# Optimization experiments

Hardware: AMD Instinct MI355X
Metric: run time of the kernel (lower is better)

## Reference

```python
import jax, jax.numpy as jnp
import numpy as np


def fps(p, m):
    """Furthest point sampling. p: (B,N,3) -> idx (B,m) int32. Starts at index 0 like pointops."""
    p = jax.lax.stop_gradient(p)
    B, N, _ = p.shape
    d2 = jnp.full((B, N), jnp.inf, dtype=p.dtype)  # min sq-dist to selected set
    first = jnp.zeros((B,), dtype=jnp.int32)

    def step(carry, _):
        d2, last = carry
        lastp = jnp.take_along_axis(p, last[:, None, None].astype(jnp.int32), axis=1)  # (B,1,3)
        dist = jnp.sum((p - lastp) ** 2, axis=-1)  # (B,N)
        d2 = jnp.minimum(d2, dist)
        nxt = jnp.argmax(d2, axis=-1).astype(jnp.int32)
        return (d2, nxt), last

    _, idx = jax.lax.scan(step, (d2, first), None, length=m)
    return jnp.transpose(idx)  # (B,m)


def knn_indices(p1, p2, k):
    """k nearest neighbors of p2 (B,M,3) among p1 (B,N,3) -> (B,M,k) int32."""
    p1 = jax.lax.stop_gradient(p1)
    p2 = jax.lax.stop_gradient(p2)
    # squared distances (B,M,N)
    d2 = (jnp.sum(p2 ** 2, -1)[:, :, None]
          + jnp.sum(p1 ** 2, -1)[:, None, :]
          - 2.0 * jnp.einsum('bmd,bnd->bmn', p2, p1))
    _, idx = jax.lax.top_k(-d2, k)
    return idx.astype(jnp.int32)


def setup_inputs() -> dict:
    key = jax.random.key(0)
    k1, k2 = jax.random.split(key)
    B, N, C = 8, 8192, 64
    p1 = jax.random.normal(k1, (B, N, 3), dtype=jnp.float32)
    x = jax.random.normal(k2, (B, N, C), dtype=jnp.float32)
    return {"p1": p1, "x": x, "stride": 4, "num_neighbors": 16}


def reference(p1, x, stride, num_neighbors):
    B, N, C = x.shape
    M = N // stride
    idx = fps(p1, M)                                   # (B,M) int32
    p2 = jnp.take_along_axis(p1, idx[:, :, None], 1)   # (B,M,3) sampled coords
    nn = knn_indices(p1, p2, num_neighbors)            # (B,M,k)
    # gather features: (B,M,k,C)
    grouped = jax.vmap(lambda xb, ib: xb[ib])(x, nn)
    y = jnp.mean(grouped, axis=2)                      # (B,M,C)
    return (y, p2, idx)
```

## Files before the change

### kernel.cpp

```cpp
#include <hip/hip_runtime.h>

#define Bn 8
#define Nn 8192
#define Cn 64
#define Mn 2048
#define Kn 16
#define FPS_T 512
#define PPT (Nn / FPS_T)

template <int CTRL, int RMASK>
__device__ __forceinline__ float dpp_max_step(float v) {
    int mv = __builtin_amdgcn_update_dpp(__float_as_int(v), __float_as_int(v),
                                         CTRL, RMASK, 0xF, false);
    return fmaxf(v, __int_as_float(mv));
}
template <int CTRL, int RMASK>
__device__ __forceinline__ unsigned dpp_min_step(unsigned v) {
    unsigned mv = (unsigned)__builtin_amdgcn_update_dpp((int)v, (int)v,
                                                        CTRL, RMASK, 0xF, false);
    return (mv < v) ? mv : v;
}
__device__ __forceinline__ float wave_max_f32(float v) {
    v = dpp_max_step<0x111, 0xF>(v);
    v = dpp_max_step<0x112, 0xF>(v);
    v = dpp_max_step<0x114, 0xF>(v);
    v = dpp_max_step<0x118, 0xF>(v);
    v = dpp_max_step<0x142, 0xA>(v);
    v = dpp_max_step<0x143, 0xC>(v);
    return v;
}
__device__ __forceinline__ unsigned wave_min_u32(unsigned v) {
    v = dpp_min_step<0x111, 0xF>(v);
    v = dpp_min_step<0x112, 0xF>(v);
    v = dpp_min_step<0x114, 0xF>(v);
    v = dpp_min_step<0x118, 0xF>(v);
    v = dpp_min_step<0x142, 0xA>(v);
    v = dpp_min_step<0x143, 0xC>(v);
    return v;
}

__global__ __launch_bounds__(FPS_T) void fps_kernel(
    const float* __restrict__ p1,
    float* __restrict__ out_p2,
    float* __restrict__ out_idxf)
{
    __shared__ float s_Px[Nn], s_Py[Nn], s_Pz[Nn];
    __shared__ unsigned long long s_key[3];
    __shared__ int s_oidx[Mn];

    const int b = blockIdx.x;
    const int t = threadIdx.x;
    const float* __restrict__ P = p1 + (size_t)b * (Nn * 3);

    float px[PPT], py[PPT], pz[PPT], d2[PPT];
#pragma unroll
    for (int j = 0; j < PPT; ++j) {
        const int g = t + j * FPS_T;
        const float x = P[g * 3 + 0];
        const float y = P[g * 3 + 1];
        const float z = P[g * 3 + 2];
        px[j] = x; py[j] = y; pz[j] = z;
        s_Px[g] = x; s_Py[g] = y; s_Pz[g] = z;
        d2[j] = __int_as_float(0x7f800000);
    }
    if (t < 3) s_key[t] = 0ull;
    if (t == 0) s_oidx[0] = 0;
    __syncthreads();

    float qx = s_Px[0], qy = s_Py[0], qz = s_Pz[0];

    for (int m = 1; m < Mn; ++m) {
        float lm = -1.0f;
#pragma unroll
        for (int j = 0; j < PPT; ++j) {
            const float dx = __fsub_rn(px[j], qx);
            const float dy = __fsub_rn(py[j], qy);
            const float dz = __fsub_rn(pz[j], qz);
            const float dist = __fadd_rn(
                __fadd_rn(__fmul_rn(dx, dx), __fmul_rn(dy, dy)),
                __fmul_rn(dz, dz));
            const float nd = fminf(d2[j], dist);
            d2[j] = nd;
            lm = fmaxf(lm, nd);
        }
        lm = wave_max_f32(lm);
        const float V = __int_as_float(
            __builtin_amdgcn_readlane(__float_as_int(lm), 63));
        unsigned cand = 0xFFFFFFFFu;
#pragma unroll
        for (int j = PPT - 1; j >= 0; --j)
            cand = (d2[j] == V) ? (unsigned)(t + j * FPS_T) : cand;
        cand = wave_min_u32(cand);
        if ((t & 63) == 63) {
            const unsigned long long key =
                ((unsigned long long)(unsigned)__float_as_int(V) << 32) |
                (unsigned long long)(~cand);
            atomicMax(&s_key[m % 3], key);
        }
        if (t == 0) s_key[(m + 1) % 3] = 0ull;
        __syncthreads();
        const unsigned long long key = s_key[m % 3];
        const int bi = (int)(~(unsigned)key);
        if (t == 0) s_oidx[m] = bi;
        qx = s_Px[bi]; qy = s_Py[bi]; qz = s_Pz[bi];
    }
    __syncthreads();

    float* __restrict__ o2 = out_p2 + (size_t)b * Mn * 3;
    float* __restrict__ oi = out_idxf + (size_t)b * Mn;
    for (int i = t; i < Mn; i += FPS_T) {
        const int bi = s_oidx[i];
        oi[i] = (float)bi;
        o2[i * 3 + 0] = s_Px[bi];
        o2[i * 3 + 1] = s_Py[bi];
        o2[i * 3 + 2] = s_Pz[bi];
    }
}

#define KNN_WPB 4
__global__ __launch_bounds__(64 * KNN_WPB) void knn_mean_kernel(
    const float* __restrict__ p1,
    const float* __restrict__ x,
    const float* __restrict__ p2,
    float* __restrict__ y)
{
    const int lane = threadIdx.x & 63;
    const int wid  = threadIdx.x >> 6;
    const int q    = blockIdx.x * KNN_WPB + wid;
    const int b    = q >> 11;
    const float* __restrict__ P = p1 + (size_t)b * (Nn * 3);

    const float qx = p2[(size_t)q * 3 + 0];
    const float qy = p2[(size_t)q * 3 + 1];
    const float qz = p2[(size_t)q * 3 + 2];
    const float qq = __fadd_rn(
        __fadd_rn(__fmul_rn(qx, qx), __fmul_rn(qy, qy)), __fmul_rn(qz, qz));

    float slotv = __int_as_float(0x7f800000);
    int   sloti = 0x7fffffff;
    float thr   = __int_as_float(0x7f800000);
    int   thri  = 0x7fffffff;

    for (int c = 0; c < Nn / 64; ++c) {
        const int g = c * 64 + lane;
        const float ax = P[g * 3 + 0];
        const float ay = P[g * 3 + 1];
        const float az = P[g * 3 + 2];
        const float pp = __fadd_rn(
            __fadd_rn(__fmul_rn(ax, ax), __fmul_rn(ay, ay)), __fmul_rn(az, az));
        const float dot = __fmaf_rn(az, qz, __fmaf_rn(ay, qy, __fmul_rn(ax, qx)));
        const float d = __fsub_rn(__fadd_rn(qq, pp), __fmul_rn(2.0f, dot));
        const bool pass = (d < thr) || (d == thr && g < thri);
        unsigned long long ball = __ballot(pass);
        while (ball) {
            const int src = __builtin_ctzll(ball);
            ball &= ball - 1ull;
            const float v  = __shfl(d, src);
            const int   vi = __shfl(g, src);
            const float upv = __shfl_up(slotv, 1);
            const int   upi = __shfl_up(sloti, 1);
            const bool beforeme = (v < slotv) || (v == slotv && vi < sloti);
            bool beforeup = (v < upv) || (v == upv && vi < upi);
            if (lane == 0) beforeup = false;
            if (beforeme) {
                slotv = beforeup ? upv : v;
                sloti = beforeup ? upi : vi;
            }
            thr  = __shfl(slotv, 15);
            thri = __shfl(sloti, 15);
        }
    }

    float acc = 0.0f;
    const float* __restrict__ xb = x + (size_t)b * Nn * Cn;
#pragma unroll
    for (int s = 0; s < Kn; ++s) {
        const int ni = __shfl(sloti, s);
        acc = __fadd_rn(acc, xb[(size_t)ni * Cn + lane]);
    }
    y[(size_t)q * Cn + lane] = __fmul_rn(acc, 0.0625f);
}

extern "C" void kernel_launch(void* const* d_in, const int* in_sizes, int n_in,
                              void* d_out, int out_size, void* d_ws, size_t ws_size,
                              hipStream_t stream) {
    const float* p1 = (const float*)d_in[0];
    const float* x  = (const float*)d_in[1];

    float* y    = (float*)d_out;
    float* p2   = y    + (size_t)Bn * Mn * Cn;
    float* idxf = p2   + (size_t)Bn * Mn * 3;

    fps_kernel<<<Bn, FPS_T, 0, stream>>>(p1, p2, idxf);
    knn_mean_kernel<<<(Bn * Mn) / KNN_WPB, 64 * KNN_WPB, 0, stream>>>(p1, x, p2, y);
}
```

Baseline: 2.122 ms.

## Pack FPS distance math into float2 vectors and replace LDS atomics with per-wave keys

```diff
diff --git a/kernel.cpp b/kernel.cpp
--- a/kernel.cpp
+++ b/kernel.cpp
@@ -7,6 +7,10 @@
 #define Kn 16
 #define FPS_T 512
 #define PPT (Nn / FPS_T)
+#define NPAIR (PPT / 2)
+
+typedef float f32x2 __attribute__((ext_vector_type(2)));
+typedef unsigned long long u64;
 
 template <int CTRL, int RMASK>
 __device__ __forceinline__ float dpp_max_step(float v) {
@@ -38,69 +42,87 @@
     v = dpp_min_step<0x143, 0xC>(v);
     return v;
 }
+__device__ __forceinline__ u64 u64max(u64 a, u64 b) { return a > b ? a : b; }
 
 __global__ __launch_bounds__(FPS_T) void fps_kernel(
     const float* __restrict__ p1,
     float* __restrict__ out_p2,
     float* __restrict__ out_idxf)
 {
+#pragma clang fp contract(off)
     __shared__ float s_Px[Nn], s_Py[Nn], s_Pz[Nn];
-    __shared__ unsigned long long s_key[3];
+    __shared__ u64 s_wkey[2][8];
     __shared__ int s_oidx[Mn];
 
     const int b = blockIdx.x;
     const int t = threadIdx.x;
+    const int w = t >> 6;
     const float* __restrict__ P = p1 + (size_t)b * (Nn * 3);
 
-    float px[PPT], py[PPT], pz[PPT], d2[PPT];
+    f32x2 px2[NPAIR], py2[NPAIR], pz2[NPAIR], d2v[NPAIR];
 #pragma unroll
     for (int j = 0; j < PPT; ++j) {
         const int g = t + j * FPS_T;
         const float x = P[g * 3 + 0];
         const float y = P[g * 3 + 1];
         const float z = P[g * 3 + 2];
-        px[j] = x; py[j] = y; pz[j] = z;
+        const int k = j >> 1;
+        if ((j & 1) == 0) { px2[k].x = x; py2[k].x = y; pz2[k].x = z; d2v[k].x = __int_as_float(0x7f800000); }
+        else              { px2[k].y = x; py2[k].y = y; pz2[k].y = z; d2v[k].y = __int_as_float(0x7f800000); }
         s_Px[g] = x; s_Py[g] = y; s_Pz[g] = z;
-        d2[j] = __int_as_float(0x7f800000);
-    }
-    if (t < 3) s_key[t] = 0ull;
+    }
     if (t == 0) s_oidx[0] = 0;
     __syncthreads();
 
     float qx = s_Px[0], qy = s_Py[0], qz = s_Pz[0];
 
     for (int m = 1; m < Mn; ++m) {
+#pragma clang fp contract(off)
+        const f32x2 nqx = { -qx, -qx };
+        const f32x2 nqy = { -qy, -qy };
+        const f32x2 nqz = { -qz, -qz };
         float lm = -1.0f;
 #pragma unroll
-        for (int j = 0; j < PPT; ++j) {
-            const float dx = __fsub_rn(px[j], qx);
-            const float dy = __fsub_rn(py[j], qy);
-            const float dz = __fsub_rn(pz[j], qz);
-            const float dist = __fadd_rn(
-                __fadd_rn(__fmul_rn(dx, dx), __fmul_rn(dy, dy)),
-                __fmul_rn(dz, dz));
-            const float nd = fminf(d2[j], dist);
-            d2[j] = nd;
-            lm = fmaxf(lm, nd);
+        for (int k = 0; k < NPAIR; ++k) {
+            const f32x2 dx = px2[k] + nqx;
+            const f32x2 dy = py2[k] + nqy;
+            const f32x2 dz = pz2[k] + nqz;
+            const f32x2 mx = dx * dx;
+            const f32x2 my = dy * dy;
+            const f32x2 mz = dz * dz;
+            const f32x2 s  = (mx + my) + mz;
+            const float nlo = fminf(d2v[k].x, s.x);
+            const float nhi = fminf(d2v[k].y, s.y);
+            d2v[k].x = nlo;
+            d2v[k].y = nhi;
+            lm = fmaxf(lm, nlo);
+            lm = fmaxf(lm, nhi);
         }
         lm = wave_max_f32(lm);
         const float V = __int_as_float(
             __builtin_amdgcn_readlane(__float_as_int(lm), 63));
         unsigned cand = 0xFFFFFFFFu;
 #pragma unroll
-        for (int j = PPT - 1; j >= 0; --j)
-            cand = (d2[j] == V) ? (unsigned)(t + j * FPS_T) : cand;
+        for (int k = NPAIR - 1; k >= 0; --k) {
+            const unsigned ghi = (unsigned)(t + (2 * k + 1) * FPS_T);
+            const unsigned glo = (unsigned)(t + (2 * k) * FPS_T);
+            cand = (d2v[k].y == V) ? ghi : cand;
+            cand = (d2v[k].x == V) ? glo : cand;
+        }
         cand = wave_min_u32(cand);
         if ((t & 63) == 63) {
-            const unsigned long long key =
-                ((unsigned long long)(unsigned)__float_as_int(V) << 32) |
-                (unsigned long long)(~cand);
-            atomicMax(&s_key[m % 3], key);
-        }
-        if (t == 0) s_key[(m + 1) % 3] = 0ull;
+            const u64 key = ((u64)(unsigned)__float_as_int(V) << 32) |
+                            (u64)(~cand);
+            s_wkey[m & 1][w] = key;
+        }
         __syncthreads();
-        const unsigned long long key = s_key[m % 3];
-        const int bi = (int)(~(unsigned)key);
+        const u64* __restrict__ K = s_wkey[m & 1];
+        const u64 a0 = u64max(K[0], K[1]);
+        const u64 a1 = u64max(K[2], K[3]);
+        const u64 a2 = u64max(K[4], K[5]);
+        const u64 a3 = u64max(K[6], K[7]);
+        const u64 kk = u64max(u64max(a0, a1), u64max(a2, a3));
+        const int bi = (int)(~(unsigned)kk);
         if (t == 0) s_oidx[m] = bi;
         qx = s_Px[bi]; qy = s_Py[bi]; qz = s_Pz[bi];
     }
```

Result: no change. 2.117 ms (median of 2 runs) (-0.2%).
